# Optimization experiments

Measured on AMD Instinct MI355X. Metric: run time of the kernel, lower is better.

The kernel has to match this reference:

```python
import jax, jax.numpy as jnp
import numpy as np

N, E, G = 100000, 1600000, 2000
D_IN, D_H, D_MLP, D_OUT = 768, 128, 32, 2


def setup_inputs() -> dict:
    key = jax.random.key(0)
    ks = jax.random.split(key, 12)
    x = jax.random.normal(ks[0], (N, D_IN), dtype=jnp.float32)
    edge_index = jax.random.randint(ks[1], (2, E), 0, N, dtype=jnp.int64)
    edge_attr = jax.random.uniform(ks[2], (E, 1), dtype=jnp.float32)
    batch = jnp.sort(jax.random.randint(ks[3], (N,), 0, G, dtype=jnp.int64))
    s1 = 1.0 / np.sqrt(D_IN)
    s2 = 1.0 / np.sqrt(D_H)
    s3 = 1.0 / np.sqrt(D_MLP)
    return {
        "x": x, "edge_index": edge_index, "edge_attr": edge_attr,
        "batch": batch, "num_graphs": G,
        "W1i": jax.random.normal(ks[4], (D_IN, D_H), dtype=jnp.float32) * s1,
        "W1r": jax.random.normal(ks[5], (D_IN, D_H), dtype=jnp.float32) * s1,
        "b1": jnp.zeros((D_H,), dtype=jnp.float32),
        "W2i": jax.random.normal(ks[6], (D_H, D_H), dtype=jnp.float32) * s2,
        "W2r": jax.random.normal(ks[7], (D_H, D_H), dtype=jnp.float32) * s2,
        "b2": jnp.zeros((D_H,), dtype=jnp.float32),
        "Wl1": jax.random.normal(ks[8], (D_H, D_MLP), dtype=jnp.float32) * s2,
        "bl1": jnp.zeros((D_MLP,), dtype=jnp.float32),
        "Wl2": jax.random.normal(ks[9], (D_MLP, D_OUT), dtype=jnp.float32) * s3,
        "bl2": jnp.zeros((D_OUT,), dtype=jnp.float32),
    }


def _arma_conv(x, row, col, ew, Wi, Wr, b, n_nodes):
    # gcn_norm without self-loops: D^{-1/2} A D^{-1/2}
    deg = jax.ops.segment_sum(ew, col, num_segments=n_nodes)
    dinv = jnp.where(deg > 0, jax.lax.rsqrt(jnp.where(deg > 0, deg, 1.0)), 0.0)
    norm = dinv[row] * ew * dinv[col]
    h = x @ Wi                                   # [N, F_out]
    msg = h[row] * norm[:, None]                 # gather + scale  [E, F_out]
    agg = jax.ops.segment_sum(msg, col, num_segments=n_nodes)
    return jax.nn.relu(agg + x @ Wr + b)         # ARMA: K=1, T=1, act=ReLU


def reference(x, edge_index, edge_attr, batch, num_graphs,
              W1i, W1r, b1, W2i, W2r, b2, Wl1, bl1, Wl2, bl2):
    row, col = edge_index[0], edge_index[1]
    ew = edge_attr.reshape(-1)
    n = x.shape[0]
    h = jax.nn.elu(_arma_conv(x, row, col, ew, W1i, W1r, b1, n))
    node_x = _arma_conv(h, row, col, ew, W2i, W2r, b2, n)
    # global mean pool over graphs
    sums = jax.ops.segment_sum(node_x, batch, num_segments=num_graphs)
    cnt = jax.ops.segment_sum(jnp.ones((n,), node_x.dtype), batch, num_segments=num_graphs)
    graph_x = sums / jnp.maximum(cnt, 1.0)[:, None]
    pred = jax.nn.elu(graph_x @ Wl1 + bl1) @ Wl2 + bl2
    return pred
```

## Files before the change

### kernel.cpp

```cpp
#include <hip/hip_runtime.h>
#include <hip/hip_bf16.h>
#include <math.h>

typedef __attribute__((ext_vector_type(8))) short short8;
typedef __attribute__((ext_vector_type(4))) float f32x4;
typedef __attribute__((address_space(1))) const void gvoid;
typedef __attribute__((address_space(3))) void lvoid;

__device__ __forceinline__ unsigned short f2bf(float f) {
    unsigned int u = __builtin_bit_cast(unsigned int, f);
    return (unsigned short)((u + 0x7fffu + ((u >> 16) & 1u)) >> 16);
}
__device__ __forceinline__ float b2f(short s) {
    return __builtin_bit_cast(float, ((unsigned int)(unsigned short)s) << 16);
}
__device__ __forceinline__ unsigned int cvtpk(float lo, float hi) {
    unsigned int r;
    asm("v_cvt_pk_bf16_f32 %0, %1, %2" : "=v"(r) : "v"(lo), "v"(hi));
    return r;
}

__global__ __launch_bounds__(256) void deg_hist_kernel(
    const int* __restrict__ ei, const float* __restrict__ ea,
    unsigned long long* __restrict__ packed, int E)
{
    int e = blockIdx.x * 256 + threadIdx.x;
    if (e >= E) return;
    int c = ei[(size_t)E + e];
    unsigned long long fx = (unsigned long long)(ea[e] * 1048576.0f + 0.5f);
    atomicAdd(&packed[c], (1ULL << 42) | fx);
}

__global__ __launch_bounds__(256) void scan1p_kernel(
    const unsigned long long* __restrict__ packed, int* __restrict__ out,
    int* __restrict__ blksum, int n)
{
    __shared__ int part[256];
    const int t = threadIdx.x;
    const int base = blockIdx.x * 1024 + t * 4;
    int v[4];
#pragma unroll
    for (int q = 0; q < 4; ++q)
        v[q] = (base + q < n) ? (int)(packed[base + q] >> 42) : 0;
    const int s = v[0] + v[1] + v[2] + v[3];
    part[t] = s;
    __syncthreads();
    for (int off = 1; off < 256; off <<= 1) {
        int x = (t >= off) ? part[t - off] : 0;
        __syncthreads();
        part[t] += x;
        __syncthreads();
    }
    if (t == 255) blksum[blockIdx.x] = part[255];
    int run = part[t] - s;
#pragma unroll
    for (int q = 0; q < 4; ++q) {
        if (base + q < n) out[base + q] = run;
        run += v[q];
    }
}

__global__ __launch_bounds__(256) void scan1_kernel(
    const int* __restrict__ in, int* __restrict__ out, int* __restrict__ blksum, int n)
{
    __shared__ int part[256];
    const int t = threadIdx.x;
    const int base = blockIdx.x * 1024 + t * 4;
    int v[4];
#pragma unroll
    for (int q = 0; q < 4; ++q) v[q] = (base + q < n) ? in[base + q] : 0;
    const int s = v[0] + v[1] + v[2] + v[3];
    part[t] = s;
    __syncthreads();
    for (int off = 1; off < 256; off <<= 1) {
        int x = (t >= off) ? part[t - off] : 0;
        __syncthreads();
        part[t] += x;
        __syncthreads();
    }
    if (t == 255) blksum[blockIdx.x] = part[255];
    int run = part[t] - s;
#pragma unroll
    for (int q = 0; q < 4; ++q) {
        if (base + q < n) out[base + q] = run;
        run += v[q];
    }
}

__global__ __launch_bounds__(256) void scan3_kernel(
    int* __restrict__ rowptr, const int* __restrict__ blkoff,
    int* __restrict__ wp, const unsigned long long* __restrict__ packed,
    float* __restrict__ dinv, int n, int Etot)
{
    int i = blockIdx.x * 256 + threadIdx.x;
    if (i == 0) rowptr[n] = Etot;
    if (i >= n) return;
    int v = rowptr[i] + blkoff[i >> 10];
    rowptr[i] = v;
    wp[i] = v;
    unsigned long long fx = packed[i] & ((1ULL << 42) - 1);
    dinv[i] = (fx > 0) ? rsqrtf((float)fx * 9.5367431640625e-7f) : 0.f;
}

__global__ __launch_bounds__(256) void place_kernel(
    const int* __restrict__ ei, const float* __restrict__ ea,
    const float* __restrict__ dinv, int* __restrict__ wp,
    int2* __restrict__ csr, int E)
{
    int e = blockIdx.x * 256 + threadIdx.x;
    if (e >= E) return;
    int r = ei[e];
    int c = ei[(size_t)E + e];
    float nm = dinv[r] * ea[e] * dinv[c];
    int p = atomicAdd(&wp[c], 1);
    int2 rec;
    rec.x = r;
    rec.y = __builtin_bit_cast(int, nm);
    csr[p] = rec;
}

__global__ __launch_bounds__(256) void conv_weights(
    const float* __restrict__ W1i, const float* __restrict__ W1r,
    const float* __restrict__ W2i, const float* __restrict__ W2r,
    unsigned short* __restrict__ W1t, unsigned short* __restrict__ W2t)
{
    int id = blockIdx.x * 256 + threadIdx.x;
    if (id < 256 * 768) {
        int n = id / 768, j = id % 768;
        int k = (j & ~63) | ((((j >> 3) & 7) ^ (n & 7)) << 3) | (j & 7);
        float v = (n < 128) ? W1i[k * 128 + n] : W1r[k * 128 + (n - 128)];
        W1t[id] = f2bf(v);
    } else {
        int id2 = id - 256 * 768;
        if (id2 < 128 * 256) {
            int n = id2 >> 8, j = id2 & 255;
            int k = (j & ~63) | ((((j >> 3) & 7) ^ (n & 7)) << 3) | (j & 7);
            float v = (k < 128) ? W2i[k * 128 + n] : W2r[(k - 128) * 128 + n];
            W2t[id2] = f2bf(v);
        }
    }
}

__global__ __launch_bounds__(512) void gemm_mfma_dual(
    const float* __restrict__ A, const unsigned short* __restrict__ Wt,
    const float* __restrict__ bias, unsigned short* __restrict__ outP,
    unsigned short* __restrict__ outR, int M, int K)
{
    __shared__ __align__(16) unsigned char As[64 * 128];
    __shared__ __align__(16) unsigned char Bs[256 * 128];

    const int t = threadIdx.x;
    const int m0 = blockIdx.x * 64;
    const int lane = t & 63;
    const int wid = t >> 6;
    const int wm = wid >> 2;
    const int wn = wid & 3;
    const int lr = lane & 15;
    const int lk = (lane >> 4) * 8;

    f32x4 acc[2][4] = {};

    const int sr = t >> 3;
    const int sk = (t & 7) * 8;
    const int aRow = m0 + sr;
    const bool aOk = (aRow < M);
    const float* aSrc = A + (size_t)(aOk ? aRow : 0) * K + sk;
    const int aDst = sr * 128 + ((sk * 2) ^ ((sr & 7) << 4));
    const unsigned short* bSrc = Wt + (size_t)(lane >> 3) * K + (lane & 7) * 8;

    for (int k0 = 0; k0 < K; k0 += 64) {
#pragma unroll
        for (int i = 0; i < 4; ++i) {
            const int chunk = i * 8 + wid;
            __builtin_amdgcn_global_load_lds(
                (gvoid*)(bSrc + (size_t)chunk * 8 * K + k0),
                (lvoid*)(Bs + chunk * 1024), 16, 0, 0);
        }
        unsigned int p0 = 0, p1 = 0, p2 = 0, p3 = 0;
        if (aOk) {
            const float4 f0 = *(const float4*)(aSrc + k0);
            const float4 f1 = *(const float4*)(aSrc + k0 + 4);
            p0 = cvtpk(f0.x, f0.y);
            p1 = cvtpk(f0.z, f0.w);
            p2 = cvtpk(f1.x, f1.y);
            p3 = cvtpk(f1.z, f1.w);
        }
        uint4 uv = {p0, p1, p2, p3};
        *(uint4*)(As + aDst) = uv;
        __syncthreads();
#pragma unroll
        for (int ks = 0; ks < 2; ++ks) {
            short8 a[2], b[4];
#pragma unroll
            for (int mf = 0; mf < 2; ++mf) {
                const int r = wm * 32 + mf * 16 + lr;
                a[mf] = *(const short8*)(As + r * 128 + (((ks * 32 + lk) * 2) ^ ((r & 7) << 4)));
            }
#pragma unroll
            for (int nf = 0; nf < 4; ++nf) {
                const int n = wn * 64 + nf * 16 + lr;
                b[nf] = *(const short8*)(Bs + n * 128 + (((ks * 32 + lk) * 2) ^ ((n & 7) << 4)));
            }
#pragma unroll
            for (int mf = 0; mf < 2; ++mf)
#pragma unroll
                for (int nf = 0; nf < 4; ++nf)
                    acc[mf][nf] = __builtin_amdgcn_mfma_f32_16x16x32_bf16(
                        a[mf], b[nf], acc[mf][nf], 0, 0, 0);
        }
        __syncthreads();
    }

#pragma unroll
    for (int mf = 0; mf < 2; ++mf) {
#pragma unroll
        for (int nf = 0; nf < 4; ++nf) {
            const int n = wn * 64 + nf * 16 + lr;
            const f32x4 v = acc[mf][nf];
            if (n < 128) {
#pragma unroll
                for (int j = 0; j < 4; ++j) {
                    const int m = m0 + wm * 32 + mf * 16 + (lane >> 4) * 4 + j;
                    if (m < M) outP[(size_t)m * 128 + n] = f2bf(v[j]);
                }
            } else {
                const int nl = n - 128;
                const float badd = bias[nl];
#pragma unroll
                for (int j = 0; j < 4; ++j) {
                    const int m = m0 + wm * 32 + mf * 16 + (lane >> 4) * 4 + j;
                    if (m < M) outR[(size_t)m * 128 + nl] = f2bf(v[j] + badd);
                }
            }
        }
    }
}

__global__ __launch_bounds__(512) void gemm_mfma_single(
    const unsigned short* __restrict__ Aa,
    const unsigned short* __restrict__ Ah,
    const unsigned short* __restrict__ Wt,
    const float* __restrict__ bias,
    unsigned short* __restrict__ outX, int M)
{
    __shared__ __align__(16) unsigned char As[128 * 128];
    __shared__ __align__(16) unsigned char Bs[128 * 128];

    const int t = threadIdx.x;
    const int m0 = blockIdx.x * 128;
    const int lane = t & 63;
    const int wid = t >> 6;
    const int wm = wid >> 1;
    const int wn = wid & 1;
    const int lr = lane & 15;
    const int lk = (lane >> 4) * 8;

    f32x4 acc[2][4] = {};

    const int sr = t >> 2;
    const int sk = (t & 3) * 16;
    const int aRow = m0 + sr;
    const bool aOk = (aRow < M);
    const int rowSafe = aOk ? aRow : 0;
    const int sw = (sr & 7) << 4;
    const unsigned short* bSrc = Wt + (size_t)(lane >> 3) * 256 + (lane & 7) * 8;

    for (int k0 = 0; k0 < 256; k0 += 64) {
#pragma unroll
        for (int i = 0; i < 2; ++i) {
            const int chunk = i * 8 + wid;
            __builtin_amdgcn_global_load_lds(
                (gvoid*)(bSrc + (size_t)chunk * 8 * 256 + k0),
                (lvoid*)(Bs + chunk * 1024), 16, 0, 0);
        }
        const unsigned short* src =
            (k0 < 128 ? Aa : Ah) + (size_t)rowSafe * 128 + (k0 & 127) + sk;
        const short8 v0 = *(const short8*)(src);
        const short8 v1 = *(const short8*)(src + 8);
        *(short8*)(As + sr * 128 + ((sk * 2) ^ sw)) = v0;
        *(short8*)(As + sr * 128 + ((sk * 2 + 16) ^ sw)) = v1;
        __syncthreads();
#pragma unroll
        for (int ks = 0; ks < 2; ++ks) {
            short8 a[2], b[4];
#pragma unroll
            for (int mf = 0; mf < 2; ++mf) {
                const int r = wm * 32 + mf * 16 + lr;
                a[mf] = *(const short8*)(As + r * 128 + (((ks * 32 + lk) * 2) ^ ((r & 7) << 4)));
            }
#pragma unroll
            for (int nf = 0; nf < 4; ++nf) {
                const int n = wn * 64 + nf * 16 + lr;
                b[nf] = *(const short8*)(Bs + n * 128 + (((ks * 32 + lk) * 2) ^ ((n & 7) << 4)));
            }
#pragma unroll
            for (int mf = 0; mf < 2; ++mf)
#pragma unroll
                for (int nf = 0; nf < 4; ++nf)
                    acc[mf][nf] = __builtin_amdgcn_mfma_f32_16x16x32_bf16(
                        a[mf], b[nf], acc[mf][nf], 0, 0, 0);
        }
        __syncthreads();
    }

#pragma unroll
    for (int mf = 0; mf < 2; ++mf) {
#pragma unroll
        for (int nf = 0; nf < 4; ++nf) {
            const int n = wn * 64 + nf * 16 + lr;
            const float bb = bias[n];
            const f32x4 v = acc[mf][nf];
#pragma unroll
            for (int j = 0; j < 4; ++j) {
                const int m = m0 + wm * 32 + mf * 16 + (lane >> 4) * 4 + j;
                if (m < M) outX[(size_t)m * 128 + n] = f2bf(fmaxf(v[j] + bb, 0.f));
            }
        }
    }
}

__global__ __launch_bounds__(256) void agg_bias_relu(
    const unsigned short* __restrict__ P, const unsigned short* __restrict__ Rbf,
    const int* __restrict__ rowptr, const int2* __restrict__ csr,
    unsigned short* __restrict__ hout, int N)
{
    const int i = blockIdx.x * 16 + (threadIdx.x >> 4);
    const int l = threadIdx.x & 15;
    if (i >= N) return;
    const int beg = rowptr[i];
    const int end = rowptr[i + 1];
    const int c = l * 8;

    float acc0[8] = {}, acc1[8] = {}, acc2[8] = {}, acc3[8] = {};
    int j = beg;
    for (; j + 3 < end; j += 4) {
        const int2 e0 = csr[j],     e1 = csr[j + 1];
        const int2 e2 = csr[j + 2], e3 = csr[j + 3];
        const short8 v0 = *(const short8*)(P + (size_t)e0.x * 128 + c);
        const short8 v1 = *(const short8*)(P + (size_t)e1.x * 128 + c);
        const short8 v2 = *(const short8*)(P + (size_t)e2.x * 128 + c);
        const short8 v3 = *(const short8*)(P + (size_t)e3.x * 128 + c);
        const float n0 = __builtin_bit_cast(float, e0.y);
        const float n1 = __builtin_bit_cast(float, e1.y);
        const float n2 = __builtin_bit_cast(float, e2.y);
        const float n3 = __builtin_bit_cast(float, e3.y);
#pragma unroll
        for (int q = 0; q < 8; ++q) {
            acc0[q] = fmaf(b2f(v0[q]), n0, acc0[q]);
            acc1[q] = fmaf(b2f(v1[q]), n1, acc1[q]);
            acc2[q] = fmaf(b2f(v2[q]), n2, acc2[q]);
            acc3[q] = fmaf(b2f(v3[q]), n3, acc3[q]);
        }
    }
    for (; j < end; ++j) {
        const int2 e0 = csr[j];
        const short8 v0 = *(const short8*)(P + (size_t)e0.x * 128 + c);
        const float n0 = __builtin_bit_cast(float, e0.y);
#pragma unroll
        for (int q = 0; q < 8; ++q) acc0[q] = fmaf(b2f(v0[q]), n0, acc0[q]);
    }
    const short8 rv = *(const short8*)(Rbf + (size_t)i * 128 + c);
    short8 ov;
#pragma unroll
    for (int q = 0; q < 8; ++q)
        ov[q] = (short)f2bf(fmaxf((acc0[q] + acc1[q]) + (acc2[q] + acc3[q]) + b2f(rv[q]), 0.f));
    *(short8*)(hout + (size_t)i * 128 + c) = ov;
}

__global__ __launch_bounds__(256) void agg_plain(
    const unsigned short* __restrict__ H,
    const int* __restrict__ rowptr, const int2* __restrict__ csr,
    unsigned short* __restrict__ ahout, int N)
{
    const int i = blockIdx.x * 16 + (threadIdx.x >> 4);
    const int l = threadIdx.x & 15;
    if (i >= N) return;
    const int beg = rowptr[i];
    const int end = rowptr[i + 1];
    const int c = l * 8;

    float acc0[8] = {}, acc1[8] = {}, acc2[8] = {}, acc3[8] = {};
    int j = beg;
    for (; j + 3 < end; j += 4) {
        const int2 e0 = csr[j],     e1 = csr[j + 1];
        const int2 e2 = csr[j + 2], e3 = csr[j + 3];
        const short8 v0 = *(const short8*)(H + (size_t)e0.x * 128 + c);
        const short8 v1 = *(const short8*)(H + (size_t)e1.x * 128 + c);
        const short8 v2 = *(const short8*)(H + (size_t)e2.x * 128 + c);
        const short8 v3 = *(const short8*)(H + (size_t)e3.x * 128 + c);
        const float n0 = __builtin_bit_cast(float, e0.y);
        const float n1 = __builtin_bit_cast(float, e1.y);
        const float n2 = __builtin_bit_cast(float, e2.y);
        const float n3 = __builtin_bit_cast(float, e3.y);
#pragma unroll
        for (int q = 0; q < 8; ++q) {
            acc0[q] = fmaf(b2f(v0[q]), n0, acc0[q]);
            acc1[q] = fmaf(b2f(v1[q]), n1, acc1[q]);
            acc2[q] = fmaf(b2f(v2[q]), n2, acc2[q]);
            acc3[q] = fmaf(b2f(v3[q]), n3, acc3[q]);
        }
    }
    for (; j < end; ++j) {
        const int2 e0 = csr[j];
        const short8 v0 = *(const short8*)(H + (size_t)e0.x * 128 + c);
        const float n0 = __builtin_bit_cast(float, e0.y);
#pragma unroll
        for (int q = 0; q < 8; ++q) acc0[q] = fmaf(b2f(v0[q]), n0, acc0[q]);
    }
    short8 ov;
#pragma unroll
    for (int q = 0; q < 8; ++q)
        ov[q] = (short)f2bf((acc0[q] + acc1[q]) + (acc2[q] + acc3[q]));
    *(short8*)(ahout + (size_t)i * 128 + c) = ov;
}

__global__ __launch_bounds__(128) void pool_mlp(
    const unsigned short* __restrict__ nx, const int* __restrict__ batch, int N,
    const float* __restrict__ Wl1, const float* __restrict__ bl1,
    const float* __restrict__ Wl2, const float* __restrict__ bl2,
    float* __restrict__ out)
{
    __shared__ float gx[128];
    __shared__ float hid[32];
    __shared__ int rng[2];
    const int g = blockIdx.x;
    const int t = threadIdx.x;
    if (t < 2) {
        const int target = g + t;
        int lo = 0, hi = N;
        while (lo < hi) {
            int mid = (lo + hi) >> 1;
            if (batch[mid] < target) lo = mid + 1; else hi = mid;
        }
        rng[t] = lo;
    }
    __syncthreads();
    const int s = rng[0], e = rng[1];
    float a0 = 0.f, a1 = 0.f, a2 = 0.f, a3 = 0.f;
    int i = s;
    for (; i + 3 < e; i += 4) {
        a0 += b2f((short)nx[(size_t)(i + 0) * 128 + t]);
        a1 += b2f((short)nx[(size_t)(i + 1) * 128 + t]);
        a2 += b2f((short)nx[(size_t)(i + 2) * 128 + t]);
        a3 += b2f((short)nx[(size_t)(i + 3) * 128 + t]);
    }
    for (; i < e; ++i) a0 += b2f((short)nx[(size_t)i * 128 + t]);
    gx[t] = ((a0 + a1) + (a2 + a3)) / fmaxf((float)(e - s), 1.f);
    __syncthreads();
    if (t < 32) {
        float a = bl1[t];
#pragma unroll 8
        for (int k = 0; k < 128; ++k) a = fmaf(gx[k], Wl1[k * 32 + t], a);
        hid[t] = a > 0.f ? a : expm1f(a);
    }
    __syncthreads();
    if (t < 2) {
        float a = bl2[t];
#pragma unroll
        for (int k = 0; k < 32; ++k) a = fmaf(hid[k], Wl2[k * 2 + t], a);
        out[(size_t)g * 2 + t] = a;
    }
}

extern "C" void kernel_launch(void* const* d_in, const int* in_sizes, int n_in,
                              void* d_out, int out_size, void* d_ws, size_t ws_size,
                              hipStream_t stream)
{
    const float* x     = (const float*)d_in[0];
    const int*   ei    = (const int*)d_in[1];
    const float* ea    = (const float*)d_in[2];
    const int*   batch = (const int*)d_in[3];
    const float* W1i   = (const float*)d_in[5];
    const float* W1r   = (const float*)d_in[6];
    const float* b1    = (const float*)d_in[7];
    const float* W2i   = (const float*)d_in[8];
    const float* W2r   = (const float*)d_in[9];
    const float* b2    = (const float*)d_in[10];
    const float* Wl1   = (const float*)d_in[11];
    const float* bl1   = (const float*)d_in[12];
    const float* Wl2   = (const float*)d_in[13];
    const float* bl2   = (const float*)d_in[14];

    const int N = in_sizes[0] / 768;
    const int E = in_sizes[2];
    const int G = out_size / 2;

    char* ws = (char*)d_ws;
    size_t off = 0;
    auto alloc = [&](size_t bytes) -> char* {
        char* p = ws + off;
        off = (off + bytes + 255) & ~(size_t)255;
        return p;
    };
    unsigned long long* packed = (unsigned long long*)alloc((size_t)N * 8);
    float* dinv    = (float*)alloc((size_t)N * 4);
    int*   rowptr  = (int*)alloc((size_t)(N + 1) * 4);
    int*   wp      = (int*)alloc((size_t)N * 4);
    int*   blkoff  = (int*)alloc((size_t)1056 * 4);
    int*   blkdum  = (int*)alloc((size_t)4 * 4);
    int2*  csr     = (int2*)alloc((size_t)E * 8);
    unsigned short* P1   = (unsigned short*)alloc((size_t)N * 128 * 2);
    unsigned short* R1   = (unsigned short*)alloc((size_t)N * 128 * 2);
    unsigned short* hbf  = (unsigned short*)alloc((size_t)N * 128 * 2);
    unsigned short* ahb  = (unsigned short*)alloc((size_t)N * 128 * 2);
    unsigned short* nxb  = (unsigned short*)alloc((size_t)N * 128 * 2);
    unsigned short* W1t  = (unsigned short*)alloc((size_t)256 * 768 * 2);
    unsigned short* W2t  = (unsigned short*)alloc((size_t)128 * 256 * 2);

    const int eBlocks = (E + 255) / 256;
    const int nb      = (N + 1023) / 1024;
    const int nBlocks = (N + 255) / 256;
    const int aBlocks = (N + 15) / 16;

    hipMemsetAsync(packed, 0, (size_t)N * 8, stream);
    deg_hist_kernel<<<eBlocks, 256, 0, stream>>>(ei, ea, packed, E);
    scan1p_kernel<<<nb, 256, 0, stream>>>(packed, rowptr, blkoff, N);
    scan1_kernel<<<1, 256, 0, stream>>>(blkoff, blkoff, blkdum, nb);
    scan3_kernel<<<nBlocks, 256, 0, stream>>>(rowptr, blkoff, wp, packed, dinv, N, E);
    place_kernel<<<eBlocks, 256, 0, stream>>>(ei, ea, dinv, wp, csr, E);
    conv_weights<<<(256 * 768 + 128 * 256 + 255) / 256, 256, 0, stream>>>(
        W1i, W1r, W2i, W2r, W1t, W2t);

    gemm_mfma_dual<<<(N + 63) / 64, 512, 0, stream>>>(x, W1t, b1, P1, R1, N, 768);
    agg_bias_relu<<<aBlocks, 256, 0, stream>>>(P1, R1, rowptr, csr, hbf, N);

    agg_plain<<<aBlocks, 256, 0, stream>>>(hbf, rowptr, csr, ahb, N);
    gemm_mfma_single<<<(N + 127) / 128, 512, 0, stream>>>(ahb, hbf, W2t, b2, nxb, N);

    pool_mlp<<<G, 128, 0, stream>>>(nxb, batch, N, Wl1, bl1, Wl2, bl2, (float*)d_out);
}
```

Measured before the change: 455.6 us.

## Privatize degree histogram, double-buffer layer-1 GEMM, split pool rows across threads

The degree histogram now spreads atomics over 8 per-block-group copies and records each edge's rank, so the CSR placement kernel computes slots directly without a second pass of atomics. The layer-1 MFMA GEMM double-buffers its A and B LDS tiles and prefetches the next K chunk while the current one is computed, removing one barrier per iteration at the cost of twice the LDS. pool_mlp uses 256 threads, with two halves summing alternating rows. These changes add memset and scan traffic for 8 copies, and the higher LDS use may reduce GEMM occupancy.

```diff
diff --git a/kernel.cpp b/kernel.cpp
--- a/kernel.cpp
+++ b/kernel.cpp
@@ -7,6 +7,8 @@
 typedef __attribute__((address_space(1))) const void gvoid;
 typedef __attribute__((address_space(3))) void lvoid;
 
+#define NC 8
+
 __device__ __forceinline__ unsigned short f2bf(float f) {
     unsigned int u = __builtin_bit_cast(unsigned int, f);
     return (unsigned short)((u + 0x7fffu + ((u >> 16) & 1u)) >> 16);
@@ -22,13 +24,15 @@
 
 __global__ __launch_bounds__(256) void deg_hist_kernel(
     const int* __restrict__ ei, const float* __restrict__ ea,
-    unsigned long long* __restrict__ packed, int E)
+    unsigned long long* __restrict__ packed, int* __restrict__ rank, int N, int E)
 {
     int e = blockIdx.x * 256 + threadIdx.x;
     if (e >= E) return;
+    const int copy = blockIdx.x & (NC - 1);
     int c = ei[(size_t)E + e];
     unsigned long long fx = (unsigned long long)(ea[e] * 1048576.0f + 0.5f);
-    atomicAdd(&packed[c], (1ULL << 42) | fx);
+    unsigned long long old = atomicAdd(&packed[(size_t)copy * N + c], (1ULL << 42) | fx);
+    rank[e] = (int)(old >> 42);
 }
 
 __global__ __launch_bounds__(256) void scan1p_kernel(
@@ -40,8 +44,15 @@
     const int base = blockIdx.x * 1024 + t * 4;
     int v[4];
 #pragma unroll
-    for (int q = 0; q < 4; ++q)
-        v[q] = (base + q < n) ? (int)(packed[base + q] >> 42) : 0;
+    for (int q = 0; q < 4; ++q) {
+        int s = 0;
+        if (base + q < n) {
+#pragma unroll
+            for (int p = 0; p < NC; ++p)
+                s += (int)(packed[(size_t)p * n + base + q] >> 42);
+        }
+        v[q] = s;
+    }
     const int s = v[0] + v[1] + v[2] + v[3];
     part[t] = s;
     __syncthreads();
@@ -89,34 +100,42 @@
 
 __global__ __launch_bounds__(256) void scan3_kernel(
     int* __restrict__ rowptr, const int* __restrict__ blkoff,
-    int* __restrict__ wp, const unsigned long long* __restrict__ packed,
+    int* __restrict__ wpb, const unsigned long long* __restrict__ packed,
     float* __restrict__ dinv, int n, int Etot)
 {
     int i = blockIdx.x * 256 + threadIdx.x;
     if (i == 0) rowptr[n] = Etot;
     if (i >= n) return;
-    int v = rowptr[i] + blkoff[i >> 10];
-    rowptr[i] = v;
-    wp[i] = v;
-    unsigned long long fx = packed[i] & ((1ULL << 42) - 1);
-    dinv[i] = (fx > 0) ? rsqrtf((float)fx * 9.5367431640625e-7f) : 0.f;
+    int base = rowptr[i] + blkoff[i >> 10];
+    rowptr[i] = base;
+    unsigned long long degfx = 0;
+    int acc = base;
+#pragma unroll
+    for (int p = 0; p < NC; ++p) {
+        unsigned long long v = packed[(size_t)p * n + i];
+        wpb[(size_t)p * n + i] = acc;
+        acc += (int)(v >> 42);
+        degfx += v & ((1ULL << 42) - 1);
+    }
+    dinv[i] = (degfx > 0) ? rsqrtf((float)degfx * 9.5367431640625e-7f) : 0.f;
 }
 
 __global__ __launch_bounds__(256) void place_kernel(
     const int* __restrict__ ei, const float* __restrict__ ea,
-    const float* __restrict__ dinv, int* __restrict__ wp,
-    int2* __restrict__ csr, int E)
+    const float* __restrict__ dinv, const int* __restrict__ wpb,
+    const int* __restrict__ rank, int2* __restrict__ csr, int N, int E)
 {
     int e = blockIdx.x * 256 + threadIdx.x;
     if (e >= E) return;
+    const int copy = blockIdx.x & (NC - 1);
     int r = ei[e];
     int c = ei[(size_t)E + e];
     float nm = dinv[r] * ea[e] * dinv[c];
-    int p = atomicAdd(&wp[c], 1);
+    int pos = wpb[(size_t)copy * N + c] + rank[e];
     int2 rec;
     rec.x = r;
     rec.y = __builtin_bit_cast(int, nm);
-    csr[p] = rec;
+    csr[pos] = rec;
 }
 
 __global__ __launch_bounds__(256) void conv_weights(
@@ -146,8 +165,8 @@
     const float* __restrict__ bias, unsigned short* __restrict__ outP,
     unsigned short* __restrict__ outR, int M, int K)
 {
-    __shared__ __align__(16) unsigned char As[64 * 128];
-    __shared__ __align__(16) unsigned char Bs[256 * 128];
+    __shared__ __align__(16) unsigned char As[2][64 * 128];
+    __shared__ __align__(16) unsigned char Bs[2][256 * 128];
 
     const int t = threadIdx.x;
     const int m0 = blockIdx.x * 64;
@@ -168,38 +187,54 @@
     const int aDst = sr * 128 + ((sk * 2) ^ ((sr & 7) << 4));
     const unsigned short* bSrc = Wt + (size_t)(lane >> 3) * K + (lane & 7) * 8;
 
+#pragma unroll
+    for (int i = 0; i < 4; ++i) {
+        const int chunk = i * 8 + wid;
+        __builtin_amdgcn_global_load_lds(
+            (gvoid*)(bSrc + (size_t)chunk * 8 * K),
+            (lvoid*)(&Bs[0][chunk * 1024]), 16, 0, 0);
+    }
+    {
+        float4 f0 = {}, f1 = {};
+        if (aOk) { f0 = *(const float4*)(aSrc); f1 = *(const float4*)(aSrc + 4); }
+        uint4 uv = {cvtpk(f0.x, f0.y), cvtpk(f0.z, f0.w),
+                    cvtpk(f1.x, f1.y), cvtpk(f1.z, f1.w)};
+        *(uint4*)(&As[0][aDst]) = uv;
+    }
+
     for (int k0 = 0; k0 < K; k0 += 64) {
-#pragma unroll
-        for (int i = 0; i < 4; ++i) {
-            const int chunk = i * 8 + wid;
-            __builtin_amdgcn_global_load_lds(
-                (gvoid*)(bSrc + (size_t)chunk * 8 * K + k0),
-                (lvoid*)(Bs + chunk * 1024), 16, 0, 0);
-        }
-        unsigned int p0 = 0, p1 = 0, p2 = 0, p3 = 0;
-        if (aOk) {
-            const float4 f0 = *(const float4*)(aSrc + k0);
-            const float4 f1 = *(const float4*)(aSrc + k0 + 4);
-            p0 = cvtpk(f0.x, f0.y);
-            p1 = cvtpk(f0.z, f0.w);
-            p2 = cvtpk(f1.x, f1.y);
-            p3 = cvtpk(f1.z, f1.w);
-        }
-        uint4 uv = {p0, p1, p2, p3};
-        *(uint4*)(As + aDst) = uv;
-        __syncthreads();
+        const int cur = (k0 >> 6) & 1;
+        const int nxt = cur ^ 1;
+        const bool hasNext = (k0 + 64 < K);
+        __syncthreads();
+
+        float4 g0 = {}, g1 = {};
+        if (hasNext) {
+#pragma unroll
+            for (int i = 0; i < 4; ++i) {
+                const int chunk = i * 8 + wid;
+                __builtin_amdgcn_global_load_lds(
+                    (gvoid*)(bSrc + (size_t)chunk * 8 * K + k0 + 64),
+                    (lvoid*)(&Bs[nxt][chunk * 1024]), 16, 0, 0);
+            }
+            if (aOk) {
+                g0 = *(const float4*)(aSrc + k0 + 64);
+                g1 = *(const float4*)(aSrc + k0 + 64 + 4);
+            }
+        }
+
 #pragma unroll
         for (int ks = 0; ks < 2; ++ks) {
             short8 a[2], b[4];
 #pragma unroll
             for (int mf = 0; mf < 2; ++mf) {
                 const int r = wm * 32 + mf * 16 + lr;
-                a[mf] = *(const short8*)(As + r * 128 + (((ks * 32 + lk) * 2) ^ ((r & 7) << 4)));
+                a[mf] = *(const short8*)(&As[cur][r * 128 + (((ks * 32 + lk) * 2) ^ ((r & 7) << 4))]);
             }
 #pragma unroll
             for (int nf = 0; nf < 4; ++nf) {
                 const int n = wn * 64 + nf * 16 + lr;
-                b[nf] = *(const short8*)(Bs + n * 128 + (((ks * 32 + lk) * 2) ^ ((n & 7) << 4)));
+                b[nf] = *(const short8*)(&Bs[cur][n * 128 + (((ks * 32 + lk) * 2) ^ ((n & 7) << 4))]);
             }
 #pragma unroll
             for (int mf = 0; mf < 2; ++mf)
@@ -208,7 +243,12 @@
                     acc[mf][nf] = __builtin_amdgcn_mfma_f32_16x16x32_bf16(
                         a[mf], b[nf], acc[mf][nf], 0, 0, 0);
         }
-        __syncthreads();
+
+        if (hasNext) {
+            uint4 uv = {cvtpk(g0.x, g0.y), cvtpk(g0.z, g0.w),
+                        cvtpk(g1.x, g1.y), cvtpk(g1.z, g1.w)};
+            *(uint4*)(&As[nxt][aDst]) = uv;
+        }
     }
 
 #pragma unroll
@@ -414,13 +454,13 @@
     *(short8*)(ahout + (size_t)i * 128 + c) = ov;
 }
 
-__global__ __launch_bounds__(128) void pool_mlp(
+__global__ __launch_bounds__(256) void pool_mlp(
     const unsigned short* __restrict__ nx, const int* __restrict__ batch, int N,
     const float* __restrict__ Wl1, const float* __restrict__ bl1,
     const float* __restrict__ Wl2, const float* __restrict__ bl2,
     float* __restrict__ out)
 {
-    __shared__ float gx[128];
+    __shared__ float gxp[2][128];
     __shared__ float hid[32];
     __shared__ int rng[2];
     const int g = blockIdx.x;
@@ -436,21 +476,25 @@
     }
     __syncthreads();
     const int s = rng[0], e = rng[1];
+    const int col = t & 127;
+    const int half = t >> 7;
     float a0 = 0.f, a1 = 0.f, a2 = 0.f, a3 = 0.f;
-    int i = s;
-    for (; i + 3 < e; i += 4) {
-        a0 += b2f((short)nx[(size_t)(i + 0) * 128 + t]);
-        a1 += b2f((short)nx[(size_t)(i + 1) * 128 + t]);
-        a2 += b2f((short)nx[(size_t)(i + 2) * 128 + t]);
-        a3 += b2f((short)nx[(size_t)(i + 3) * 128 + t]);
-    }
-    for (; i < e; ++i) a0 += b2f((short)nx[(size_t)i * 128 + t]);
-    gx[t] = ((a0 + a1) + (a2 + a3)) / fmaxf((float)(e - s), 1.f);
+    int i = s + half;
+    for (; i + 6 < e; i += 8) {
+        a0 += b2f((short)nx[(size_t)(i + 0) * 128 + col]);
+        a1 += b2f((short)nx[(size_t)(i + 2) * 128 + col]);
+        a2 += b2f((short)nx[(size_t)(i + 4) * 128 + col]);
+        a3 += b2f((short)nx[(size_t)(i + 6) * 128 + col]);
+    }
+    for (; i < e; i += 2) a0 += b2f((short)nx[(size_t)i * 128 + col]);
+    gxp[half][col] = (a0 + a1) + (a2 + a3);
+    __syncthreads();
+    if (t < 128) gxp[0][t] = (gxp[0][t] + gxp[1][t]) / fmaxf((float)(e - s), 1.f);
     __syncthreads();
     if (t < 32) {
         float a = bl1[t];
 #pragma unroll 8
-        for (int k = 0; k < 128; ++k) a = fmaf(gx[k], Wl1[k * 32 + t], a);
+        for (int k = 0; k < 128; ++k) a = fmaf(gxp[0][k], Wl1[k * 32 + t], a);
         hid[t] = a > 0.f ? a : expm1f(a);
     }
     __syncthreads();
@@ -492,10 +536,11 @@
         off = (off + bytes + 255) & ~(size_t)255;
         return p;
     };
-    unsigned long long* packed = (unsigned long long*)alloc((size_t)N * 8);
+    unsigned long long* packed = (unsigned long long*)alloc((size_t)NC * N * 8);
+    int*   rank    = (int*)alloc((size_t)E * 4);
+    int*   wpb     = (int*)alloc((size_t)NC * N * 4);
     float* dinv    = (float*)alloc((size_t)N * 4);
     int*   rowptr  = (int*)alloc((size_t)(N + 1) * 4);
-    int*   wp      = (int*)alloc((size_t)N * 4);
     int*   blkoff  = (int*)alloc((size_t)1056 * 4);
     int*   blkdum  = (int*)alloc((size_t)4 * 4);
     int2*  csr     = (int2*)alloc((size_t)E * 8);
@@ -512,12 +557,12 @@
     const int nBlocks = (N + 255) / 256;
     const int aBlocks = (N + 15) / 16;
 
-    hipMemsetAsync(packed, 0, (size_t)N * 8, stream);
-    deg_hist_kernel<<<eBlocks, 256, 0, stream>>>(ei, ea, packed, E);
+    hipMemsetAsync(packed, 0, (size_t)NC * N * 8, stream);
+    deg_hist_kernel<<<eBlocks, 256, 0, stream>>>(ei, ea, packed, rank, N, E);
     scan1p_kernel<<<nb, 256, 0, stream>>>(packed, rowptr, blkoff, N);
     scan1_kernel<<<1, 256, 0, stream>>>(blkoff, blkoff, blkdum, nb);
-    scan3_kernel<<<nBlocks, 256, 0, stream>>>(rowptr, blkoff, wp, packed, dinv, N, E);
-    place_kernel<<<eBlocks, 256, 0, stream>>>(ei, ea, dinv, wp, csr, E);
+    scan3_kernel<<<nBlocks, 256, 0, stream>>>(rowptr, blkoff, wpb, packed, dinv, N, E);
+    place_kernel<<<eBlocks, 256, 0, stream>>>(ei, ea, dinv, wpb, rank, csr, N, E);
     conv_weights<<<(256 * 768 + 128 * 256 + 255) / 256, 256, 0, stream>>>(
         W1i, W1r, W2i, W2r, W1t, W2t);
 
@@ -527,5 +572,5 @@
     agg_plain<<<aBlocks, 256, 0, stream>>>(hbf, rowptr, csr, ahb, N);
     gemm_mfma_single<<<(N + 127) / 128, 512, 0, stream>>>(ahb, hbf, W2t, b2, nxb, N);
 
-    pool_mlp<<<G, 128, 0, stream>>>(nxb, batch, N, Wl1, bl1, Wl2, bl2, (float*)d_out);
-}
+    pool_mlp<<<G, 256, 0, stream>>>(nxb, batch, N, Wl1, bl1, Wl2, bl2, (float*)d_out);
+}
```

Measured after the change: 430.4 us. -5.5%, faster.
